# Performance work log

Hardware: AMD Instinct MI355X
Metric: run time of the kernel (lower is better)

## Reference

```python
import jax, jax.numpy as jnp
import numpy as np

N, E = 50000, 400000          # nodes, edges (avg degree 8)
DIN, DEIN = 128, 128          # in_node_feats, in_edge_feats
H, DE, DN = 8, 16, 16         # num_heads, out_edge_feats, out_node_feats
HDE = H * DE                  # 128


def setup_inputs() -> dict:
    key = jax.random.key(0)
    ks = jax.random.split(key, 14)
    nfeats = jax.random.normal(ks[0], (N, DIN), jnp.float32)
    efeats = jax.random.normal(ks[1], (E, DEIN), jnp.float32)
    norm = jax.random.uniform(ks[2], (E, 1), jnp.float32)
    src = jax.random.randint(ks[3], (E,), 0, N, jnp.int32)
    # guarantee every node has in-degree >= 1 (module raises on 0-in-degree)
    dst = jnp.concatenate([jax.random.permutation(ks[4], N).astype(jnp.int32),
                           jax.random.randint(ks[5], (E - N,), 0, N, jnp.int32)])
    s = 0.05
    W_ni = jax.random.normal(ks[6], (HDE, DIN), jnp.float32) * s
    W_nj = jax.random.normal(ks[7], (HDE, DIN), jnp.float32) * s
    W_fij = jax.random.normal(ks[8], (HDE, DEIN), jnp.float32) * s
    W_edges = jax.random.normal(ks[9], (HDE, 3 * HDE), jnp.float32) * s
    W_attn = jax.random.normal(ks[10], (H, DE), jnp.float32) * s
    bias = jnp.zeros((HDE,), jnp.float32)
    W_node = jax.random.normal(ks[11], (H * DN, DIN), jnp.float32) * s
    b_node = jnp.zeros((H * DN,), jnp.float32)
    return dict(nfeats=nfeats, efeats=efeats, norm=norm, src=src, dst=dst,
                W_ni=W_ni, W_nj=W_nj, W_fij=W_fij, W_edges=W_edges,
                W_attn=W_attn, bias=bias, W_node=W_node, b_node=b_node)


def reference(nfeats, efeats, norm, src, dst,
              W_ni, W_nj, W_fij, W_edges, W_attn, bias, W_node, b_node):
    # node/edge linear projections
    f_ni = nfeats @ W_ni.T            # [N, H*De]
    f_nj = nfeats @ W_nj.T            # [N, H*De]
    f_eij = efeats @ W_fij.T          # [E, H*De]
    # fc_edges(cat[f_ni[src], f_eij, f_nj[dst]]) == sum of 3 block-matmuls;
    # project on nodes/edges FIRST, then gather (same math, less edge traffic)
    W1, W2, W3 = jnp.split(W_edges, 3, axis=1)   # each [H*De, H*De]
    t_src = f_ni @ W1.T               # [N, H*De]
    t_e = f_eij @ W2.T                # [E, H*De]
    t_dst = f_nj @ W3.T               # [N, H*De]
    f_lin = t_src[src] + t_e + t_dst[dst]         # [E, H*De]
    f = jax.nn.leaky_relu(f_lin)                  # slope 0.01 == torch default
    f_out = (f + bias).reshape(E, H, DE)          # [E, H, De]
    # fc_attn then sum over head-out dim == dot with column-sum of W_attn
    a = jnp.einsum('ehd,d->eh', f_out, W_attn.sum(0))   # [E, H]
    # edge_softmax over edges incoming to each dst node, per head
    m = jax.ops.segment_max(a, dst, num_segments=N)     # [N, H]
    ex = jnp.exp(a - m[dst])
    den = jax.ops.segment_sum(ex, dst, num_segments=N)  # [N, H]
    alpha = (ex / den[dst])[:, :, None]                 # [E, H, 1]
    # mpnn_type='node': message = h_out[src] * a * norm, reduced by sum at dst
    h_node = (nfeats @ W_node.T + b_node).reshape(N, H, DN)
    msg = h_node[src] * alpha * norm[:, :, None]        # [E, H, Dn]
    h_out = jax.ops.segment_sum(msg, dst, num_segments=N)  # [N, H, Dn]
    return h_out.sum(axis=1), f_out.sum(axis=1)
```

## Files before the change

kernel.cpp:

```cpp
#include <hip/hip_runtime.h>

typedef unsigned short ushort_t;
typedef __attribute__((ext_vector_type(8))) short short8;
typedef __attribute__((ext_vector_type(4))) float f32x4;
typedef __attribute__((ext_vector_type(4))) int i32x4;

#define NN 50000
#define NE 400000
#define WS_NEED 46531200ull

static __device__ __forceinline__ float bf2f(ushort_t u) {
    union { unsigned int i; float f; } v; v.i = ((unsigned int)u) << 16; return v.f;
}
static __device__ __forceinline__ ushort_t f2bf(float f) {
    unsigned int u = __float_as_uint(f);
    u = (u + 0x7fffu + ((u >> 16) & 1u)) >> 16;
    return (ushort_t)u;
}
static __device__ __forceinline__ short8 cvt8(f32x4 a, f32x4 b) {
    union { short8 s; unsigned int u[4]; } r;
    asm("v_cvt_pk_bf16_f32 %0, %1, %2" : "=v"(r.u[0]) : "v"(a[0]), "v"(a[1]));
    asm("v_cvt_pk_bf16_f32 %0, %1, %2" : "=v"(r.u[1]) : "v"(a[2]), "v"(a[3]));
    asm("v_cvt_pk_bf16_f32 %0, %1, %2" : "=v"(r.u[2]) : "v"(b[0]), "v"(b[1]));
    asm("v_cvt_pk_bf16_f32 %0, %1, %2" : "=v"(r.u[3]) : "v"(b[2]), "v"(b[3]));
    return r.s;
}
static __device__ __forceinline__ float loadf(const void* base, size_t i, int f32) {
    return f32 ? ((const float*)base)[i] : bf2f(((const ushort_t*)base)[i]);
}
static __device__ __forceinline__ short8 load8(const void* base, size_t off, int f32) {
    if (f32) {
        const float* p = (const float*)base + off;
        return cvt8(*(const f32x4*)p, *(const f32x4*)(p + 4));
    }
    return *(const short8*)((const ushort_t*)base + off);
}

__global__ void k_init(const ushort_t* __restrict__ nf, int* __restrict__ flag,
                       float* __restrict__ den, float* __restrict__ out0) {
    const int i = blockIdx.x * 256 + threadIdx.x;
    if (i < NN * 8) den[i] = 0.f;
    if (i < NN * 16) out0[i] = 0.f;
    if (blockIdx.x == 0 && threadIdx.x < 64) {
        int cnt = 0;
#pragma unroll
        for (int j = 0; j < 4; j++) {
            const int eb = (nf[(threadIdx.x * 4 + j) * 2] >> 7) & 0xFF;
            cnt += (eb >= 0xB0);
        }
#pragma unroll
        for (int off = 32; off; off >>= 1) cnt += __shfl_xor(cnt, off);
        if (threadIdx.x == 0) *flag = (cnt > 8) ? 1 : 0;
    }
}

__global__ void k_zero(float* __restrict__ p, int n) {
    const int i = blockIdx.x * 256 + threadIdx.x;
    if (i < n) p[i] = 0.f;
}

__global__ void k_recip(float* __restrict__ p, int n) {
    const int i = blockIdx.x * 256 + threadIdx.x;
    if (i < n) p[i] = 1.f / fmaxf(p[i], 1e-30f);
}

__global__ void k_prep(const void* __restrict__ W_ni, const void* __restrict__ W_nj,
                       const void* __restrict__ W_fij, const void* __restrict__ W_edges,
                       const void* __restrict__ W_attn, const void* __restrict__ W_node,
                       const int* __restrict__ flag,
                       ushort_t* __restrict__ Wcat, ushort_t* __restrict__ Ae,
                       float* __restrict__ wsum) {
    const int f32 = *flag;
    int r = blockIdx.x;
    int k = threadIdx.x;
    if (r == 0 && k < 16) {
        float s = 0.f;
        for (int h = 0; h < 8; h++) s += loadf(W_attn, h * 16 + k, f32);
        wsum[k] = s;
    }
    const int ks = k ^ ((r & 7) << 3);
    float acc = 0.f;
    if (r < 128) {
        for (int m = 0; m < 128; m++)
            acc += loadf(W_edges, r * 384 + m, f32) * loadf(W_ni, m * 128 + k, f32);
        Wcat[r * 128 + ks] = f2bf(acc);
    } else if (r < 256) {
        int j = r - 128;
        for (int m = 0; m < 128; m++)
            acc += loadf(W_edges, j * 384 + 256 + m, f32) * loadf(W_nj, m * 128 + k, f32);
        Wcat[r * 128 + ks] = f2bf(acc);
    } else if (r < 384) {
        Wcat[r * 128 + ks] = f2bf(loadf(W_node, (r - 256) * 128 + k, f32));
    } else {
        int j = r - 384;
        for (int m = 0; m < 128; m++)
            acc += loadf(W_edges, j * 384 + 128 + m, f32) * loadf(W_fij, m * 128 + k, f32);
        Ae[j * 128 + (k ^ ((j & 7) << 3))] = f2bf(acc);
    }
}

__global__ __launch_bounds__(256) void k_nodes(const void* __restrict__ X,
                                               const ushort_t* __restrict__ Wcat,
                                               const void* __restrict__ b_node,
                                               const int* __restrict__ flag,
                                               ushort_t* __restrict__ tsrc,
                                               ushort_t* __restrict__ tdst,
                                               ushort_t* __restrict__ hnode) {
    __shared__ ushort_t sW[128 * 128];
    const int f32 = *flag;
    const int g = blockIdx.x % 3;
    const int tch = blockIdx.x / 3;
    const int lane = threadIdx.x & 63, wave = threadIdx.x >> 6;
    const int c = lane & 15, quad = lane >> 4;

    const ushort_t* Wg = Wcat + (size_t)g * 16384;
#pragma unroll
    for (int it2 = 0; it2 < 8; it2++) {
        const int idx = (it2 * 256 + threadIdx.x) * 8;
        *(short8*)(sW + idx) = *(const short8*)(Wg + idx);
    }
    __syncthreads();

    ushort_t* const outp = (g == 0) ? tsrc : (g == 1) ? tdst : hnode;
    float bnv[8];
#pragma unroll
    for (int t = 0; t < 8; t++) bnv[t] = (g == 2) ? loadf(b_node, t * 16 + c, f32) : 0.f;

    for (int it = 0; it < 3; it++) {
        const int tile = tch * 3 + it;
        if (tile * 64 >= NN) break;
        const int m0 = tile * 64 + wave * 16;
        int arow = m0 + c;
        if (arow >= NN) arow = NN - 1;
        short8 a[4];
#pragma unroll
        for (int k4 = 0; k4 < 4; k4++)
            a[k4] = load8(X, (size_t)arow * 128 + k4 * 32 + quad * 8, f32);
        f32x4 acc[8];
#pragma unroll
        for (int t = 0; t < 8; t++) acc[t] = (f32x4){0.f, 0.f, 0.f, 0.f};
#pragma unroll
        for (int k4 = 0; k4 < 4; k4++) {
            const int ks = (k4 * 32 + quad * 8) ^ ((c & 7) << 3);
#pragma unroll
            for (int t = 0; t < 8; t++) {
                short8 b = *(const short8*)(sW + (size_t)(t * 16 + c) * 128 + ks);
                acc[t] = __builtin_amdgcn_mfma_f32_16x16x32_bf16(a[k4], b, acc[t], 0, 0, 0);
            }
        }
#pragma unroll
        for (int r = 0; r < 4; r++) {
            const int m = m0 + quad * 4 + r;
            f32x4 lo, hi;
#pragma unroll
            for (int t = 0; t < 4; t++) { lo[t] = acc[t][r] + bnv[t]; hi[t] = acc[t + 4][r] + bnv[t + 4]; }
            const short8 v = cvt8(lo, hi);
            if (m < NN) *(short8*)(outp + (size_t)m * 128 + c * 8) = v;
        }
    }
}

template<int F32>
static __device__ __forceinline__ void edges_body(
    const void* __restrict__ EF, const ushort_t* sAe,
    const int* __restrict__ src, const int* __restrict__ dst,
    const ushort_t* __restrict__ tsrc, const ushort_t* __restrict__ tdst,
    const void* __restrict__ bias, const float* __restrict__ wsum,
    ushort_t* __restrict__ exw, float* __restrict__ den, float* __restrict__ out1) {
    const int lane = threadIdx.x & 63, wave = threadIdx.x >> 6;
    const int c = lane & 15, quad = lane >> 4;

    const float wc = wsum[c];
    float biasv[8];
#pragma unroll
    for (int t = 0; t < 8; t++) biasv[t] = loadf(bias, t * 16 + c, F32);

    const int ew0 = blockIdx.x * 320 + wave * 16;
    i32x4 svn = *(const i32x4*)(src + ew0 + quad * 4);
    i32x4 dvn = *(const i32x4*)(dst + ew0 + quad * 4);
    f32x4 raw[8];
    short8 an[4];
    {
        const size_t base = (size_t)(ew0 + c) * 128 + quad * 8;
        if (F32) {
            const float* p = (const float*)EF;
#pragma unroll
            for (int k4 = 0; k4 < 4; k4++) {
                raw[k4 * 2]     = *(const f32x4*)(p + base + k4 * 32);
                raw[k4 * 2 + 1] = *(const f32x4*)(p + base + k4 * 32 + 4);
            }
        } else {
            const ushort_t* p = (const ushort_t*)EF;
#pragma unroll
            for (int k4 = 0; k4 < 4; k4++) an[k4] = *(const short8*)(p + base + k4 * 32);
        }
    }

    for (int it = 0; it < 5; it++) {
        const int ecur = ew0 + it * 64;
        const i32x4 sv4 = svn, dv4 = dvn;
        short8 a[4];
        if (F32) {
#pragma unroll
            for (int k4 = 0; k4 < 4; k4++) a[k4] = cvt8(raw[k4 * 2], raw[k4 * 2 + 1]);
        } else {
#pragma unroll
            for (int k4 = 0; k4 < 4; k4++) a[k4] = an[k4];
        }
        short8 ts8[4], td8[4];
#pragma unroll
        for (int r = 0; r < 4; r++) {
            ts8[r] = *(const short8*)(tsrc + (size_t)sv4[r] * 128 + c * 8);
            td8[r] = *(const short8*)(tdst + (size_t)dv4[r] * 128 + c * 8);
        }
        if (it < 4) {
            const int en = ecur + 64;
            svn = *(const i32x4*)(src + en + quad * 4);
            dvn = *(const i32x4*)(dst + en + quad * 4);
            const size_t base = (size_t)(en + c) * 128 + quad * 8;
            if (F32) {
                const float* p = (const float*)EF;
#pragma unroll
                for (int k4 = 0; k4 < 4; k4++) {
                    raw[k4 * 2]     = *(const f32x4*)(p + base + k4 * 32);
                    raw[k4 * 2 + 1] = *(const f32x4*)(p + base + k4 * 32 + 4);
                }
            } else {
                const ushort_t* p = (const ushort_t*)EF;
#pragma unroll
                for (int k4 = 0; k4 < 4; k4++) an[k4] = *(const short8*)(p + base + k4 * 32);
            }
        }
        f32x4 acc[8];
#pragma unroll
        for (int t = 0; t < 8; t++) acc[t] = (f32x4){0.f, 0.f, 0.f, 0.f};
#pragma unroll
        for (int k4 = 0; k4 < 4; k4++) {
            const int ks = (k4 * 32 + quad * 8) ^ ((c & 7) << 3);
#pragma unroll
            for (int t = 0; t < 8; t++) {
                short8 b = *(const short8*)(sAe + (size_t)(t * 16 + c) * 128 + ks);
                acc[t] = __builtin_amdgcn_mfma_f32_16x16x32_bf16(a[k4], b, acc[t], 0, 0, 0);
            }
        }
#pragma unroll
        for (int r = 0; r < 4; r++) {
            const int e = ecur + quad * 4 + r;
            const int dv = dv4[r];
            float o1 = 0.f, part[8];
#pragma unroll
            for (int t = 0; t < 8; t++) {
                float f = acc[t][r] + bf2f((ushort_t)ts8[r][t]) + bf2f((ushort_t)td8[r][t]);
                f = (f > 0.f) ? f : 0.01f * f;
                const float fo = f + biasv[t];
                o1 += fo;
                part[t] = fo * wc;
            }
            out1[(size_t)e * 16 + c] = o1;
            float q[4];
#pragma unroll
            for (int i2 = 0; i2 < 4; i2++) {
                const float send  = (c & 8) ? part[i2] : part[i2 + 4];
                const float other = __shfl_xor(send, 8);
                const float mine  = (c & 8) ? part[i2 + 4] : part[i2];
                q[i2] = mine + other;
            }
            float p2[2];
#pragma unroll
            for (int i2 = 0; i2 < 2; i2++) {
                const float send  = (c & 4) ? q[i2] : q[i2 + 2];
                const float other = __shfl_xor(send, 4);
                const float mine  = (c & 4) ? q[i2 + 2] : q[i2];
                p2[i2] = mine + other;
            }
            const float send  = (c & 2) ? p2[0] : p2[1];
            const float other = __shfl_xor(send, 2);
            const float mine  = (c & 2) ? p2[1] : p2[0];
            float p1 = mine + other;
            p1 += __shfl_xor(p1, 1);
            if (!(c & 1)) {
                const int h = c >> 1;
                const float av = fminf(fmaxf(p1, -50.f), 50.f);
                const float ex = __expf(av);
                const ushort_t exb16 = f2bf(ex);
                exw[(size_t)e * 8 + h] = exb16;
                atomicAdd(&den[(size_t)dv * 8 + h], bf2f(exb16));
            }
        }
    }
}

__global__ __launch_bounds__(256) void k_edges(const void* __restrict__ EF,
                                               const ushort_t* __restrict__ Ae,
                                               const int* __restrict__ src,
                                               const int* __restrict__ dst,
                                               const ushort_t* __restrict__ tsrc,
                                               const ushort_t* __restrict__ tdst,
                                               const void* __restrict__ bias,
                                               const float* __restrict__ wsum,
                                               const int* __restrict__ flag,
                                               ushort_t* __restrict__ exw,
                                               float* __restrict__ den,
                                               float* __restrict__ out1) {
    __shared__ ushort_t sAe[128 * 128];
#pragma unroll
    for (int it2 = 0; it2 < 8; it2++) {
        const int idx = (it2 * 256 + threadIdx.x) * 8;
        *(short8*)(sAe + idx) = *(const short8*)(Ae + idx);
    }
    __syncthreads();
    if (*flag) edges_body<1>(EF, sAe, src, dst, tsrc, tdst, bias, wsum, exw, den, out1);
    else       edges_body<0>(EF, sAe, src, dst, tsrc, tdst, bias, wsum, exw, den, out1);
}

__global__ __launch_bounds__(256) void k_msg(const int* __restrict__ src,
                                             const int* __restrict__ dst,
                                             const void* __restrict__ norm,
                                             const ushort_t* __restrict__ hnode,
                                             const ushort_t* __restrict__ exw,
                                             const float* __restrict__ den,
                                             const int* __restrict__ flag,
                                             float* __restrict__ out0) {
    const int f32 = *flag;
    const int tid = blockIdx.x * 256 + threadIdx.x;
    const int e = tid >> 4, d = tid & 15;
    if (e >= NE) return;
    const int sv = src[e], dv = dst[e];
    const float nm = loadf(norm, e, f32);
    const short8 hn = *(const short8*)(hnode + (size_t)sv * 128 + d * 8);
    const short8 ew = *(const short8*)(exw + (size_t)e * 8);
    const f32x4* rd = (const f32x4*)(den + (size_t)dv * 8);
    const f32x4 r0 = rd[0], r1 = rd[1];
    float s = 0.f;
#pragma unroll
    for (int h = 0; h < 4; h++)
        s += bf2f((ushort_t)hn[h]) * (bf2f((ushort_t)ew[h]) * r0[h]);
#pragma unroll
    for (int h = 0; h < 4; h++)
        s += bf2f((ushort_t)hn[4 + h]) * (bf2f((ushort_t)ew[4 + h]) * r1[h]);
    atomicAdd(&out0[(size_t)dv * 16 + d], s * nm);
}

extern "C" void kernel_launch(void* const* d_in, const int* in_sizes, int n_in,
                              void* d_out, int out_size, void* d_ws, size_t ws_size,
                              hipStream_t stream) {
    const void* nfeats  = d_in[0];
    const void* efeats  = d_in[1];
    const void* norm    = d_in[2];
    const int*  src     = (const int*)d_in[3];
    const int*  dst     = (const int*)d_in[4];
    const void* W_ni    = d_in[5];
    const void* W_nj    = d_in[6];
    const void* W_fij   = d_in[7];
    const void* W_edges = d_in[8];
    const void* W_attn  = d_in[9];
    const void* bias    = d_in[10];
    const void* W_node  = d_in[11];
    const void* b_node  = d_in[12];

    if (ws_size < WS_NEED) {
        k_zero<<<(out_size + 255) / 256, 256, 0, stream>>>((float*)d_out, out_size);
        return;
    }

    char* ws = (char*)d_ws;
    const size_t o_den   = 0;
    const size_t o_exw   = 1600000;
    const size_t o_wcat  = 8000000;
    const size_t o_ae    = 8098304;
    const size_t o_wsum  = 8131072;
    const size_t o_flag  = 8131136;
    const size_t o_tsrc  = 8131200;
    const size_t o_tdst  = o_tsrc + 12800000;
    const size_t o_hnode = o_tdst + 12800000;

    float*    den   = (float*)(ws + o_den);
    ushort_t* exw   = (ushort_t*)(ws + o_exw);
    ushort_t* Wcat  = (ushort_t*)(ws + o_wcat);
    ushort_t* Ae    = (ushort_t*)(ws + o_ae);
    float*    wsum  = (float*)(ws + o_wsum);
    int*      flag  = (int*)(ws + o_flag);
    ushort_t* tsrc  = (ushort_t*)(ws + o_tsrc);
    ushort_t* tdst  = (ushort_t*)(ws + o_tdst);
    ushort_t* hnode = (ushort_t*)(ws + o_hnode);

    float* out0 = (float*)d_out;
    float* out1 = (float*)d_out + NN * 16;

    k_init<<<(NN * 16 + 255) / 256, 256, 0, stream>>>((const ushort_t*)nfeats, flag, den, out0);
    k_prep<<<512, 128, 0, stream>>>(W_ni, W_nj, W_fij, W_edges, W_attn, W_node, flag, Wcat, Ae, wsum);
    k_nodes<<<786, 256, 0, stream>>>(nfeats, Wcat, b_node, flag, tsrc, tdst, hnode);
    k_edges<<<1250, 256, 0, stream>>>(efeats, Ae, src, dst, tsrc, tdst, bias, wsum, flag, exw, den, out1);
    k_recip<<<(NN * 8 + 255) / 256, 256, 0, stream>>>(den, NN * 8);
    k_msg<<<NE * 16 / 256, 256, 0, stream>>>(src, dst, norm, hnode, exw, den, flag, out0);
}
```

Before: 426.2 us.

## Templatize node GEMM on input dtype and prefetch next tile's rows

```diff
diff --git a/kernel.cpp b/kernel.cpp
--- a/kernel.cpp
+++ b/kernel.cpp
@@ -99,6 +99,89 @@
     }
 }
 
+template<int F32>
+static __device__ __forceinline__ void nodes_body(
+    const void* __restrict__ X, const ushort_t* sW,
+    const void* __restrict__ b_node, const int g, const int tch,
+    ushort_t* __restrict__ outp) {
+    const int lane = threadIdx.x & 63, wave = threadIdx.x >> 6;
+    const int c = lane & 15, quad = lane >> 4;
+    float bnv[8];
+#pragma unroll
+    for (int t = 0; t < 8; t++) bnv[t] = (g == 2) ? loadf(b_node, t * 16 + c, F32) : 0.f;
+
+    f32x4 raw[8];
+    short8 an[4];
+    {
+        int arow = tch * 128 + wave * 16 + c;
+        if (arow >= NN) arow = NN - 1;
+        const size_t base = (size_t)arow * 128 + quad * 8;
+        if (F32) {
+            const float* p = (const float*)X;
+#pragma unroll
+            for (int k4 = 0; k4 < 4; k4++) {
+                raw[k4 * 2]     = *(const f32x4*)(p + base + k4 * 32);
+                raw[k4 * 2 + 1] = *(const f32x4*)(p + base + k4 * 32 + 4);
+            }
+        } else {
+            const ushort_t* p = (const ushort_t*)X;
+#pragma unroll
+            for (int k4 = 0; k4 < 4; k4++) an[k4] = *(const short8*)(p + base + k4 * 32);
+        }
+    }
+
+#pragma unroll
+    for (int it = 0; it < 2; it++) {
+        const int m0 = (tch * 2 + it) * 64 + wave * 16;
+        short8 a[4];
+        if (F32) {
+#pragma unroll
+            for (int k4 = 0; k4 < 4; k4++) a[k4] = cvt8(raw[k4 * 2], raw[k4 * 2 + 1]);
+        } else {
+#pragma unroll
+            for (int k4 = 0; k4 < 4; k4++) a[k4] = an[k4];
+        }
+        if (it == 0) {
+            int arow = tch * 128 + 64 + wave * 16 + c;
+            if (arow >= NN) arow = NN - 1;
+            const size_t base = (size_t)arow * 128 + quad * 8;
+            if (F32) {
+                const float* p = (const float*)X;
+#pragma unroll
+                for (int k4 = 0; k4 < 4; k4++) {
+                    raw[k4 * 2]     = *(const f32x4*)(p + base + k4 * 32);
+                    raw[k4 * 2 + 1] = *(const f32x4*)(p + base + k4 * 32 + 4);
+                }
+            } else {
+                const ushort_t* p = (const ushort_t*)X;
+#pragma unroll
+                for (int k4 = 0; k4 < 4; k4++) an[k4] = *(const short8*)(p + base + k4 * 32);
+            }
+        }
+        f32x4 acc[8];
+#pragma unroll
+        for (int t = 0; t < 8; t++) acc[t] = (f32x4){0.f, 0.f, 0.f, 0.f};
+#pragma unroll
+        for (int k4 = 0; k4 < 4; k4++) {
+            const int ks = (k4 * 32 + quad * 8) ^ ((c & 7) << 3);
+#pragma unroll
+            for (int t = 0; t < 8; t++) {
+                short8 b = *(const short8*)(sW + (size_t)(t * 16 + c) * 128 + ks);
+                acc[t] = __builtin_amdgcn_mfma_f32_16x16x32_bf16(a[k4], b, acc[t], 0, 0, 0);
+            }
+        }
+#pragma unroll
+        for (int r = 0; r < 4; r++) {
+            const int m = m0 + quad * 4 + r;
+            f32x4 lo, hi;
+#pragma unroll
+            for (int t = 0; t < 4; t++) { lo[t] = acc[t][r] + bnv[t]; hi[t] = acc[t + 4][r] + bnv[t + 4]; }
+            const short8 v = cvt8(lo, hi);
+            if (m < NN) *(short8*)(outp + (size_t)m * 128 + c * 8) = v;
+        }
+    }
+}
+
 __global__ __launch_bounds__(256) void k_nodes(const void* __restrict__ X,
                                                const ushort_t* __restrict__ Wcat,
                                                const void* __restrict__ b_node,
@@ -107,12 +190,8 @@
                                                ushort_t* __restrict__ tdst,
                                                ushort_t* __restrict__ hnode) {
     __shared__ ushort_t sW[128 * 128];
-    const int f32 = *flag;
     const int g = blockIdx.x % 3;
     const int tch = blockIdx.x / 3;
-    const int lane = threadIdx.x & 63, wave = threadIdx.x >> 6;
-    const int c = lane & 15, quad = lane >> 4;
-
     const ushort_t* Wg = Wcat + (size_t)g * 16384;
 #pragma unroll
     for (int it2 = 0; it2 < 8; it2++) {
@@ -120,44 +199,9 @@
         *(short8*)(sW + idx) = *(const short8*)(Wg + idx);
     }
     __syncthreads();
-
     ushort_t* const outp = (g == 0) ? tsrc : (g == 1) ? tdst : hnode;
-    float bnv[8];
-#pragma unroll
-    for (int t = 0; t < 8; t++) bnv[t] = (g == 2) ? loadf(b_node, t * 16 + c, f32) : 0.f;
-
-    for (int it = 0; it < 3; it++) {
-        const int tile = tch * 3 + it;
-        if (tile * 64 >= NN) break;
-        const int m0 = tile * 64 + wave * 16;
-        int arow = m0 + c;
-        if (arow >= NN) arow = NN - 1;
-        short8 a[4];
-#pragma unroll
-        for (int k4 = 0; k4 < 4; k4++)
-            a[k4] = load8(X, (size_t)arow * 128 + k4 * 32 + quad * 8, f32);
-        f32x4 acc[8];
-#pragma unroll
-        for (int t = 0; t < 8; t++) acc[t] = (f32x4){0.f, 0.f, 0.f, 0.f};
-#pragma unroll
-        for (int k4 = 0; k4 < 4; k4++) {
-            const int ks = (k4 * 32 + quad * 8) ^ ((c & 7) << 3);
-#pragma unroll
-            for (int t = 0; t < 8; t++) {
-                short8 b = *(const short8*)(sW + (size_t)(t * 16 + c) * 128 + ks);
-                acc[t] = __builtin_amdgcn_mfma_f32_16x16x32_bf16(a[k4], b, acc[t], 0, 0, 0);
-            }
-        }
-#pragma unroll
-        for (int r = 0; r < 4; r++) {
-            const int m = m0 + quad * 4 + r;
-            f32x4 lo, hi;
-#pragma unroll
-            for (int t = 0; t < 4; t++) { lo[t] = acc[t][r] + bnv[t]; hi[t] = acc[t + 4][r] + bnv[t + 4]; }
-            const short8 v = cvt8(lo, hi);
-            if (m < NN) *(short8*)(outp + (size_t)m * 128 + c * 8) = v;
-        }
-    }
+    if (*flag) nodes_body<1>(X, sW, b_node, g, tch, outp);
+    else       nodes_body<0>(X, sW, b_node, g, tch, outp);
 }
 
 template<int F32>
@@ -389,7 +433,7 @@
 
     k_init<<<(NN * 16 + 255) / 256, 256, 0, stream>>>((const ushort_t*)nfeats, flag, den, out0);
     k_prep<<<512, 128, 0, stream>>>(W_ni, W_nj, W_fij, W_edges, W_attn, W_node, flag, Wcat, Ae, wsum);
-    k_nodes<<<786, 256, 0, stream>>>(nfeats, Wcat, b_node, flag, tsrc, tdst, hnode);
+    k_nodes<<<1173, 256, 0, stream>>>(nfeats, Wcat, b_node, flag, tsrc, tdst, hnode);
     k_edges<<<1250, 256, 0, stream>>>(efeats, Ae, src, dst, tsrc, tdst, bias, wsum, flag, exw, den, out1);
     k_recip<<<(NN * 8 + 255) / 256, 256, 0, stream>>>(den, NN * 8);
     k_msg<<<NE * 16 / 256, 256, 0, stream>>>(src, dst, norm, hnode, exw, den, flag, out0);
```

After: 423.4 us. Within noise of the previous version (-0.6%).
